# Kernel optimization log

Measured on AMD Instinct MI355X. Metric: run time of the kernel, lower is better.

## Reference

```python
import jax, jax.numpy as jnp
import numpy as np

N, E, G, H = 5000, 50000, 8, 4
GAT_DIMS = [(1536, 1024), (1024, 512), (512, 256)]
MLP_DIMS = [(256, 128), (128, 64), (64, 32), (32, 16), (16, 1)]
GATE_DIMS = [(256, 128), (128, 1)]
NEG_SLOPE = 0.2
EPS = 1e-16


def setup_inputs() -> dict:
    key = jax.random.key(0)
    keys = iter(jax.random.split(key, 80))

    def nrm(shape, s=0.05):
        return jax.random.normal(next(keys), shape, jnp.float32) * s

    inp = {}
    inp["x"] = jax.random.normal(next(keys), (N, 1536), jnp.float32)
    inp["edge_index"] = jax.random.randint(next(keys), (2, E), 0, N)
    inp["batch"] = jnp.sort(jax.random.randint(next(keys), (N,), 0, G))
    for i, (di, do) in enumerate(GAT_DIMS, 1):
        inp[f"Wl{i}"] = nrm((di, H * do))
        inp[f"bl{i}"] = jnp.zeros((H * do,), jnp.float32)
        inp[f"Wr{i}"] = nrm((di, H * do))
        inp[f"br{i}"] = jnp.zeros((H * do,), jnp.float32)
        inp[f"att{i}"] = nrm((H, do))
        inp[f"b{i}"] = jnp.zeros((do,), jnp.float32)
    for i, (di, do) in enumerate(MLP_DIMS):
        inp[f"Wm{i}"] = nrm((di, do))
        inp[f"bm{i}"] = jnp.zeros((do,), jnp.float32)
    for i, (di, do) in enumerate(GATE_DIMS):
        inp[f"Wg{i}"] = nrm((di, do))
        inp[f"bg{i}"] = jnp.zeros((do,), jnp.float32)
    return inp


def _gatv2(x, src, dst, Wl, bl, Wr, br, att, bias):
    # PyG GATv2Conv, concat=False: mean over heads.
    C = att.shape[1]
    xl = (x @ Wl + bl).reshape(-1, H, C)  # source-side transform [N,H,C]
    xr = (x @ Wr + br).reshape(-1, H, C)  # target-side transform [N,H,C]
    # edge scores: att . leaky_relu(x_j + x_i)  -> [E',H]
    s = jnp.sum(jax.nn.leaky_relu(xl[src] + xr[dst], negative_slope=NEG_SLOPE) * att, axis=-1)
    # segment softmax over destination node neighborhoods
    m = jax.ops.segment_max(s, dst, num_segments=N)
    ex = jnp.exp(s - m[dst])
    den = jax.ops.segment_sum(ex, dst, num_segments=N)
    alpha = ex / (den[dst] + EPS)
    out = jax.ops.segment_sum(alpha[:, :, None] * xl[src], dst, num_segments=N)  # [N,H,C]
    return out.mean(axis=1) + bias


def _forward(x, edge_index, batch, params):
    loop = jnp.arange(N)
    src = jnp.concatenate([edge_index[0], loop])  # add_self_loops=True (PyG default)
    dst = jnp.concatenate([edge_index[1], loop])
    for i in (1, 2, 3):
        x = jax.nn.relu(_gatv2(x, src, dst,
                               params[f"Wl{i}"], params[f"bl{i}"],
                               params[f"Wr{i}"], params[f"br{i}"],
                               params[f"att{i}"], params[f"b{i}"]))
    # AttentionalAggregation: segment-softmax(gate_nn(x)) weighted sum over graphs
    gate = jax.nn.relu(x @ params["Wg0"] + params["bg0"]) @ params["Wg1"] + params["bg1"]
    g = gate[:, 0]
    m = jax.ops.segment_max(g, batch, num_segments=G)
    ex = jnp.exp(g - m[batch])
    den = jax.ops.segment_sum(ex, batch, num_segments=G)
    w = ex / (den[batch] + EPS)
    h = jax.ops.segment_sum(w[:, None] * x, batch, num_segments=G)  # [G,256]
    for i in range(4):
        h = jax.nn.relu(h @ params[f"Wm{i}"] + params[f"bm{i}"])
    return h @ params["Wm4"] + params["bm4"]  # [G,1]


def reference(x, edge_index, batch,
              Wl1, bl1, Wr1, br1, att1, b1,
              Wl2, bl2, Wr2, br2, att2, b2,
              Wl3, bl3, Wr3, br3, att3, b3,
              Wm0, bm0, Wm1, bm1, Wm2, bm2, Wm3, bm3, Wm4, bm4,
              Wg0, bg0, Wg1, bg1):
    params = dict(locals())
    for k in ("x", "edge_index", "batch"):
        params.pop(k)
    return _forward(x, edge_index, batch, params)
```

## Files before the change

kernel.cpp:

```cpp
#include <hip/hip_runtime.h>
#include <math.h>

#define NN 5000
#define NNP 5120
#define NE 50000
#define NEE 55000
#define NG 8
#define NH 4

typedef __attribute__((ext_vector_type(8))) _Float16 half8;
typedef __attribute__((ext_vector_type(4))) _Float16 half4;
typedef __attribute__((ext_vector_type(4))) float floatx4;


__device__ inline float waveSum(float v) {
    #pragma unroll
    for (int o = 32; o > 0; o >>= 1) v += __shfl_xor(v, o, 64);
    return v;
}
__device__ inline float waveMax(float v) {
    #pragma unroll
    for (int o = 32; o > 0; o >>= 1) v = fmaxf(v, __shfl_xor(v, o, 64));
    return v;
}

__device__ __forceinline__ void gload_lds16(const _Float16* g, _Float16* l) {
    __builtin_amdgcn_global_load_lds(
        (__attribute__((address_space(1))) void*)g,
        (__attribute__((address_space(3))) void*)l,
        16, 0, 0);
}


__global__ void k_cvtA(const float* __restrict__ X, _Float16* __restrict__ A0, int n) {
    int i = blockIdx.x * 256 + threadIdx.x;
    if (i >= n) return;
    A0[i] = (_Float16)X[i];
}

__global__ __launch_bounds__(256) void k_cvtWT(const float* __restrict__ W,
        _Float16* __restrict__ B0, int K, int M)
{
    __shared__ float tile[32][33];
    int m0 = blockIdx.x * 32, k0 = blockIdx.y * 32;
    int tx = threadIdx.x & 31, ty = threadIdx.x >> 5;
    #pragma unroll
    for (int i = 0; i < 4; ++i)
        tile[ty + 8 * i][tx] = W[(size_t)(k0 + ty + 8 * i) * M + m0 + tx];
    __syncthreads();
    #pragma unroll
    for (int i = 0; i < 4; ++i) {
        int mm = ty + 8 * i, kk = tx;
        B0[(size_t)(m0 + mm) * K + kk + k0] = (_Float16)tile[kk][mm];
    }
}

__global__ __launch_bounds__(256) void gemm_mfma_f16(
    const _Float16* __restrict__ A0, const _Float16* __restrict__ B0,
    const float* __restrict__ bias, _Float16* __restrict__ C,
    int Mrows, int K, int N)
{
    __shared__ __align__(16) _Float16 As[2][128 * 32];
    __shared__ __align__(16) _Float16 Bs[2][128 * 32];

    const int tid = threadIdx.x;
    const int wave = tid >> 6;
    const int lane = tid & 63;
    const int wm = (wave >> 1) * 64;
    const int wn = (wave & 1) * 64;
    const int lm = lane & 15;
    const int kq = (lane >> 4) * 8;
    const int rowBase = blockIdx.y * 128;
    const int colBase = blockIdx.x * 128;

    floatx4 acc[4][4];
    #pragma unroll
    for (int i = 0; i < 4; ++i)
        #pragma unroll
        for (int j = 0; j < 4; ++j)
            acc[i][j] = (floatx4){0.f, 0.f, 0.f, 0.f};

    const int srow = wave * 32 + (lane >> 2);
    const int scol = (lane & 3) * 8;
    const _Float16* gA = A0 + (size_t)(rowBase + srow) * K + scol;
    const _Float16* gB = B0 + (size_t)(colBase + srow) * K + scol;
    const size_t rowSkip = (size_t)16 * K;
    const int lo0 = (wave * 32) * 32;
    const int lo1 = (wave * 32 + 16) * 32;

    gload_lds16(gA, &As[0][lo0]);
    gload_lds16(gA + rowSkip, &As[0][lo1]);
    gload_lds16(gB, &Bs[0][lo0]);
    gload_lds16(gB + rowSkip, &Bs[0][lo1]);
    __syncthreads();

    const int nk = K >> 5;
    for (int t = 0; t < nk; ++t) {
        const int p = t & 1;
        if (t + 1 < nk) {
            const int k1 = (t + 1) << 5;
            gload_lds16(gA + k1, &As[p ^ 1][lo0]);
            gload_lds16(gA + rowSkip + k1, &As[p ^ 1][lo1]);
            gload_lds16(gB + k1, &Bs[p ^ 1][lo0]);
            gload_lds16(gB + rowSkip + k1, &Bs[p ^ 1][lo1]);
        }
        half8 a0[4], b0[4];
        #pragma unroll
        for (int i = 0; i < 4; ++i) {
            a0[i] = *(const half8*)&As[p][(wm + i * 16 + lm) * 32 + kq];
            b0[i] = *(const half8*)&Bs[p][(wn + i * 16 + lm) * 32 + kq];
        }
        #pragma unroll
        for (int i = 0; i < 4; ++i)
            #pragma unroll
            for (int j = 0; j < 4; ++j)
                acc[i][j] = __builtin_amdgcn_mfma_f32_16x16x32_f16(a0[i], b0[j], acc[i][j], 0, 0, 0);
        __syncthreads();
    }

    const int cq = (lane >> 4) * 4;
    #pragma unroll
    for (int j = 0; j < 4; ++j) {
        int col = colBase + wn + j * 16 + lm;
        float bv = bias[col];
        #pragma unroll
        for (int i = 0; i < 4; ++i) {
            #pragma unroll
            for (int r = 0; r < 4; ++r) {
                int grow = rowBase + wm + i * 16 + cq + r;
                if (grow < Mrows)
                    C[(size_t)grow * N + col] = (_Float16)(acc[i][j][r] + bv);
            }
        }
    }
}


__global__ void k_build_edges(const int* __restrict__ ei, int* __restrict__ src,
                              int* __restrict__ dst) {
    int i = blockIdx.x * 256 + threadIdx.x;
    if (i < NE) { src[i] = ei[i]; dst[i] = ei[NE + i]; }
    else if (i < NEE) { src[i] = i - NE; dst[i] = i - NE; }
}

__global__ void k_zero32(unsigned int* __restrict__ p, int n) {
    int i = blockIdx.x * 256 + threadIdx.x;
    if (i < n) p[i] = 0u;
}

__global__ void k_count(const int* __restrict__ dst, int* __restrict__ cnt) {
    int i = blockIdx.x * 256 + threadIdx.x;
    if (i < NEE) atomicAdd(&cnt[dst[i]], 1);
}

__global__ __launch_bounds__(256) void k_scan(const int* __restrict__ cnt,
                                              int* __restrict__ off, int* __restrict__ cur) {
    __shared__ int partial[256];
    __shared__ int ppre[257];
    int t = threadIdx.x;
    const int chunk = (NN + 255) / 256;
    int lo = t * chunk, hi = min(NN, (t + 1) * chunk);
    int s = 0;
    for (int i = lo; i < hi; ++i) s += cnt[i];
    partial[t] = s;
    __syncthreads();
    if (t == 0) {
        int acc = 0;
        for (int i = 0; i < 256; ++i) { ppre[i] = acc; acc += partial[i]; }
        ppre[256] = acc;
    }
    __syncthreads();
    int acc = ppre[t];
    for (int i = lo; i < hi; ++i) { off[i] = acc; cur[i] = acc; acc += cnt[i]; }
    if (t == 0) off[NN] = ppre[256];
}

__global__ void k_fill(const int* __restrict__ src, const int* __restrict__ dst,
                       int* __restrict__ cur, int* __restrict__ slist) {
    int e = blockIdx.x * 256 + threadIdx.x;
    if (e < NEE) { int p = atomicAdd(&cur[dst[e]], 1); slist[p] = src[e]; }
}

template<int C>
__global__ __launch_bounds__(256) void k_gat_fused(
    const _Float16* __restrict__ xl, const _Float16* __restrict__ xr,
    const float* __restrict__ att, const int* __restrict__ eoff,
    const int* __restrict__ slist, const float* __restrict__ bias,
    _Float16* __restrict__ out)
{
    constexpr int NQ = C / 256;
    __shared__ float red[NH * C];
    const int n = blockIdx.x;
    const int h = threadIdx.x >> 6;
    const int lane = threadIdx.x & 63;

    float4 xr_reg[NQ], att_reg[NQ], acc[NQ];
    {
        const _Float16* xrow = xr + (size_t)n * (NH * C) + h * C;
        const float* ah   = att + h * C;
        #pragma unroll
        for (int q = 0; q < NQ; ++q) {
            int off = q * 256 + lane * 4;
            half4 hv = *(const half4*)(xrow + off);
            xr_reg[q] = make_float4((float)hv[0], (float)hv[1], (float)hv[2], (float)hv[3]);
            att_reg[q] = *(const float4*)(ah + off);
            acc[q] = make_float4(0.f, 0.f, 0.f, 0.f);
        }
    }
    float m = -INFINITY, den = 0.f;
    const int start = eoff[n], end = eoff[n + 1];

    for (int j = start; j < end; ++j) {
        int s = slist[j];
        const _Float16* xlr = xl + (size_t)s * (NH * C) + h * C;
        float4 xv[NQ];
        float ps = 0.f;
        #pragma unroll
        for (int q = 0; q < NQ; ++q) {
            half4 hv = *(const half4*)(xlr + q * 256 + lane * 4);
            xv[q] = make_float4((float)hv[0], (float)hv[1], (float)hv[2], (float)hv[3]);
            float vx = xv[q].x + xr_reg[q].x;
            float vy = xv[q].y + xr_reg[q].y;
            float vz = xv[q].z + xr_reg[q].z;
            float vw = xv[q].w + xr_reg[q].w;
            vx = vx > 0.f ? vx : 0.2f * vx;
            vy = vy > 0.f ? vy : 0.2f * vy;
            vz = vz > 0.f ? vz : 0.2f * vz;
            vw = vw > 0.f ? vw : 0.2f * vw;
            ps = fmaf(vx, att_reg[q].x, ps);
            ps = fmaf(vy, att_reg[q].y, ps);
            ps = fmaf(vz, att_reg[q].z, ps);
            ps = fmaf(vw, att_reg[q].w, ps);
        }
        ps = waveSum(ps);
        float m_new = fmaxf(m, ps);
        float scale = expf(m - m_new);
        float ex = expf(ps - m_new);
        den = den * scale + ex;
        m = m_new;
        #pragma unroll
        for (int q = 0; q < NQ; ++q) {
            acc[q].x = fmaf(ex, xv[q].x, acc[q].x * scale);
            acc[q].y = fmaf(ex, xv[q].y, acc[q].y * scale);
            acc[q].z = fmaf(ex, xv[q].z, acc[q].z * scale);
            acc[q].w = fmaf(ex, xv[q].w, acc[q].w * scale);
        }
    }

    float inv = 1.f / (den + 1e-16f);
    #pragma unroll
    for (int q = 0; q < NQ; ++q) {
        int off = q * 256 + lane * 4;
        float4 r;
        r.x = acc[q].x * inv; r.y = acc[q].y * inv;
        r.z = acc[q].z * inv; r.w = acc[q].w * inv;
        *(float4*)&red[h * C + off] = r;
    }
    __syncthreads();

    int t = threadIdx.x;
    for (int c4 = t; c4 < C / 4; c4 += 256) {
        int c = c4 * 4;
        float4 r0 = *(const float4*)&red[0 * C + c];
        float4 r1 = *(const float4*)&red[1 * C + c];
        float4 r2 = *(const float4*)&red[2 * C + c];
        float4 r3 = *(const float4*)&red[3 * C + c];
        float4 bv = *(const float4*)(bias + c);
        half4 o;
        o[0] = (_Float16)fmaxf((r0.x + r1.x + r2.x + r3.x) * 0.25f + bv.x, 0.f);
        o[1] = (_Float16)fmaxf((r0.y + r1.y + r2.y + r3.y) * 0.25f + bv.y, 0.f);
        o[2] = (_Float16)fmaxf((r0.z + r1.z + r2.z + r3.z) * 0.25f + bv.z, 0.f);
        o[3] = (_Float16)fmaxf((r0.w + r1.w + r2.w + r3.w) * 0.25f + bv.w, 0.f);
        *(half4*)(out + (size_t)n * C + c) = o;
    }
}


__global__ __launch_bounds__(128) void k_gate(
    const _Float16* __restrict__ x, const float* __restrict__ Wg0,
    const float* __restrict__ bg0, const float* __restrict__ Wg1,
    const float* __restrict__ bg1, float* __restrict__ g)
{
    int n = blockIdx.x;
    int t = threadIdx.x;
    __shared__ float xs[256];
    __shared__ float wsum[2];
    const _Float16* xp = x + (size_t)n * 256;
    xs[t] = (float)xp[t]; xs[t + 128] = (float)xp[t + 128];
    __syncthreads();
    float acc = bg0[t];
    for (int k = 0; k < 256; ++k) acc = fmaf(xs[k], Wg0[k * 128 + t], acc);
    acc = acc > 0.f ? acc : 0.f;
    float prod = acc * Wg1[t];
    prod = waveSum(prod);
    if ((t & 63) == 0) wsum[t >> 6] = prod;
    __syncthreads();
    if (t == 0) g[n] = wsum[0] + wsum[1] + bg1[0];
}

__global__ void k_group_bounds(const int* __restrict__ batch, int* __restrict__ gstart,
                               int* __restrict__ gend) {
    int n = blockIdx.x * 256 + threadIdx.x;
    if (n >= NN) return;
    int b = batch[n];
    if (n == 0 || batch[n - 1] != b) gstart[b] = n;
    if (n == NN - 1 || batch[n + 1] != b) gend[b] = n + 1;
}

__global__ __launch_bounds__(256) void k_pool_stats(
    const float* __restrict__ g, const int* __restrict__ gstart,
    const int* __restrict__ gend, float* __restrict__ mOut,
    float* __restrict__ invdenOut)
{
    int gi = blockIdx.x;
    int t = threadIdx.x;
    int s0 = gstart[gi], e0 = gend[gi];
    __shared__ float red[4];
    float mx = -1e30f;
    for (int n = s0 + t; n < e0; n += 256) mx = fmaxf(mx, g[n]);
    float wm = waveMax(mx);
    if ((t & 63) == 0) red[t >> 6] = wm;
    __syncthreads();
    float m = fmaxf(fmaxf(red[0], red[1]), fmaxf(red[2], red[3]));
    __syncthreads();
    float sm = 0.f;
    for (int n = s0 + t; n < e0; n += 256) sm += expf(g[n] - m);
    sm = waveSum(sm);
    if ((t & 63) == 0) red[t >> 6] = sm;
    __syncthreads();
    if (t == 0) {
        float den = red[0] + red[1] + red[2] + red[3] + 1e-16f;
        mOut[gi] = m;
        invdenOut[gi] = 1.f / den;
    }
}

#define PCH 16
__global__ __launch_bounds__(256) void k_pool_acc(
    const _Float16* __restrict__ x, const float* __restrict__ g,
    const int* __restrict__ batch, const float* __restrict__ m,
    const float* __restrict__ invden, float* __restrict__ hpool)
{
    int base = blockIdx.x * PCH;
    int t = threadIdx.x;
    float acc = 0.f;
    int cur = -1;
    for (int i = 0; i < PCH; ++i) {
        int n = base + i;
        if (n >= NN) break;
        int b = batch[n];
        if (b != cur) {
            if (cur >= 0) atomicAdd(&hpool[cur * 256 + t], acc);
            cur = b; acc = 0.f;
        }
        float w = expf(g[n] - m[b]) * invden[b];
        acc = fmaf(w, (float)x[(size_t)n * 256 + t], acc);
    }
    if (cur >= 0) atomicAdd(&hpool[cur * 256 + t], acc);
}

__global__ __launch_bounds__(256) void k_mlp(
    const float* __restrict__ hpool,
    const float* __restrict__ Wm0, const float* __restrict__ bm0,
    const float* __restrict__ Wm1, const float* __restrict__ bm1,
    const float* __restrict__ Wm2, const float* __restrict__ bm2,
    const float* __restrict__ Wm3, const float* __restrict__ bm3,
    const float* __restrict__ Wm4, const float* __restrict__ bm4,
    float* __restrict__ out)
{
    __shared__ float bufA[8 * 256];
    __shared__ float bufB[8 * 128];
    int t = threadIdx.x;
    for (int i = t; i < 8 * 256; i += 256) bufA[i] = hpool[i];
    __syncthreads();
    for (int i = t; i < 8 * 128; i += 256) {
        int r = i >> 7, c = i & 127;
        float acc = bm0[c];
        for (int k = 0; k < 256; ++k) acc = fmaf(bufA[r * 256 + k], Wm0[k * 128 + c], acc);
        bufB[i] = fmaxf(acc, 0.f);
    }
    __syncthreads();
    for (int i = t; i < 8 * 64; i += 256) {
        int r = i >> 6, c = i & 63;
        float acc = bm1[c];
        for (int k = 0; k < 128; ++k) acc = fmaf(bufB[r * 128 + k], Wm1[k * 64 + c], acc);
        bufA[i] = fmaxf(acc, 0.f);
    }
    __syncthreads();
    for (int i = t; i < 8 * 32; i += 256) {
        int r = i >> 5, c = i & 31;
        float acc = bm2[c];
        for (int k = 0; k < 64; ++k) acc = fmaf(bufA[r * 64 + k], Wm2[k * 32 + c], acc);
        bufB[i] = fmaxf(acc, 0.f);
    }
    __syncthreads();
    for (int i = t; i < 8 * 16; i += 256) {
        int r = i >> 4, c = i & 15;
        float acc = bm3[c];
        for (int k = 0; k < 32; ++k) acc = fmaf(bufB[r * 32 + k], Wm3[k * 16 + c], acc);
        bufA[i] = fmaxf(acc, 0.f);
    }
    __syncthreads();
    if (t < 8) {
        float acc = bm4[0];
        for (int k = 0; k < 16; ++k) acc = fmaf(bufA[t * 16 + k], Wm4[k], acc);
        out[t] = acc;
    }
}


static void run_gat_layer(const _Float16* ain, int K, int C,
                          const float* Wl, const float* bl,
                          const float* Wr, const float* br,
                          const float* att, const float* bias,
                          _Float16* wb0, _Float16* xl, _Float16* xr,
                          const int* eoff, const int* slist,
                          _Float16* xout, hipStream_t stream)
{
    int HC = NH * C;
    dim3 ggrid(HC / 128, NNP / 128);
    dim3 tgrid(HC / 32, K / 32);
    k_cvtWT<<<tgrid, 256, 0, stream>>>(Wl, wb0, K, HC);
    gemm_mfma_f16<<<ggrid, 256, 0, stream>>>(ain, wb0, bl, xl, NN, K, HC);
    k_cvtWT<<<tgrid, 256, 0, stream>>>(Wr, wb0, K, HC);
    gemm_mfma_f16<<<ggrid, 256, 0, stream>>>(ain, wb0, br, xr, NN, K, HC);

    if (C == 1024)
        k_gat_fused<1024><<<NN, 256, 0, stream>>>(xl, xr, att, eoff, slist, bias, xout);
    else if (C == 512)
        k_gat_fused<512><<<NN, 256, 0, stream>>>(xl, xr, att, eoff, slist, bias, xout);
    else
        k_gat_fused<256><<<NN, 256, 0, stream>>>(xl, xr, att, eoff, slist, bias, xout);
}

extern "C" void kernel_launch(void* const* d_in, const int* in_sizes, int n_in,
                              void* d_out, int out_size, void* d_ws, size_t ws_size,
                              hipStream_t stream) {
    const float* x      = (const float*)d_in[0];
    const int* ei       = (const int*)d_in[1];
    const int* batch    = (const int*)d_in[2];
    const float* Wl1 = (const float*)d_in[3];  const float* bl1 = (const float*)d_in[4];
    const float* Wr1 = (const float*)d_in[5];  const float* br1 = (const float*)d_in[6];
    const float* att1= (const float*)d_in[7];  const float* b1  = (const float*)d_in[8];
    const float* Wl2 = (const float*)d_in[9];  const float* bl2 = (const float*)d_in[10];
    const float* Wr2 = (const float*)d_in[11]; const float* br2 = (const float*)d_in[12];
    const float* att2= (const float*)d_in[13]; const float* b2  = (const float*)d_in[14];
    const float* Wl3 = (const float*)d_in[15]; const float* bl3 = (const float*)d_in[16];
    const float* Wr3 = (const float*)d_in[17]; const float* br3 = (const float*)d_in[18];
    const float* att3= (const float*)d_in[19]; const float* b3  = (const float*)d_in[20];
    const float* Wm0 = (const float*)d_in[21]; const float* bm0 = (const float*)d_in[22];
    const float* Wm1 = (const float*)d_in[23]; const float* bm1 = (const float*)d_in[24];
    const float* Wm2 = (const float*)d_in[25]; const float* bm2 = (const float*)d_in[26];
    const float* Wm3 = (const float*)d_in[27]; const float* bm3 = (const float*)d_in[28];
    const float* Wm4 = (const float*)d_in[29]; const float* bm4 = (const float*)d_in[30];
    const float* Wg0 = (const float*)d_in[31]; const float* bg0 = (const float*)d_in[32];
    const float* Wg1 = (const float*)d_in[33]; const float* bg1 = (const float*)d_in[34];
    float* out = (float*)d_out;

    float* ws = (float*)d_ws;
    size_t o = 0;
    _Float16* xl  = (_Float16*)(ws + o); o += (size_t)NNP * 4096 / 2;
    _Float16* xr  = (_Float16*)(ws + o); o += (size_t)NNP * 4096 / 2;
    _Float16* x1  = (_Float16*)(ws + o); o += (size_t)NNP * 1024 / 2;
    _Float16* x2  = (_Float16*)(ws + o); o += (size_t)NNP * 512 / 2;
    _Float16* x3  = (_Float16*)(ws + o); o += (size_t)NNP * 256 / 2;
    _Float16* a0p = (_Float16*)(ws + o); o += (size_t)NNP * 1536 / 2;
    _Float16* wb0 = (_Float16*)(ws + o); o += (size_t)1536 * 4096 / 2;
    int* srcA    = (int*)(ws + o); o += NEE;
    int* dstA    = (int*)(ws + o); o += NEE;
    int* cnt     = (int*)(ws + o); o += NN;
    int* eoff    = (int*)(ws + o); o += NN + 1;
    int* cur     = (int*)(ws + o); o += NN;
    int* slist   = (int*)(ws + o); o += NEE;
    float* g     = ws + o; o += NN;
    int* gstart  = (int*)(ws + o); o += NG;
    int* gend    = (int*)(ws + o); o += NG;
    float* gm    = ws + o; o += NG;
    float* ginv  = ws + o; o += NG;
    float* hpool = ws + o; o += NG * 256;

    int ebB = (NEE + 255) / 256;
    k_build_edges<<<ebB, 256, 0, stream>>>(ei, srcA, dstA);
    k_zero32<<<(NN + 255) / 256, 256, 0, stream>>>((unsigned int*)cnt, NN);
    k_count<<<ebB, 256, 0, stream>>>(dstA, cnt);
    k_scan<<<1, 256, 0, stream>>>(cnt, eoff, cur);
    k_fill<<<ebB, 256, 0, stream>>>(srcA, dstA, cur, slist);

    int nA = NN * 1536;
    k_cvtA<<<(nA + 255) / 256, 256, 0, stream>>>(x, a0p, nA);

    run_gat_layer(a0p, 1536, 1024, Wl1, bl1, Wr1, br1, att1, b1,
                  wb0, xl, xr, eoff, slist, x1, stream);
    run_gat_layer(x1,  1024, 512,  Wl2, bl2, Wr2, br2, att2, b2,
                  wb0, xl, xr, eoff, slist, x2, stream);
    run_gat_layer(x2,  512,  256,  Wl3, bl3, Wr3, br3, att3, b3,
                  wb0, xl, xr, eoff, slist, x3, stream);

    k_gate<<<NN, 128, 0, stream>>>(x3, Wg0, bg0, Wg1, bg1, g);
    k_zero32<<<1, 64, 0, stream>>>((unsigned int*)gstart, 2 * NG);
    k_group_bounds<<<(NN + 255) / 256, 256, 0, stream>>>(batch, gstart, gend);
    k_pool_stats<<<NG, 256, 0, stream>>>(g, gstart, gend, gm, ginv);
    k_zero32<<<(NG * 256 + 255) / 256, 256, 0, stream>>>((unsigned int*)hpool, NG * 256);
    k_pool_acc<<<(NN + PCH - 1) / PCH, 256, 0, stream>>>(x3, g, batch, gm, ginv, hpool);
    k_mlp<<<1, 256, 0, stream>>>(hpool, Wm0, bm0, Wm1, bm1, Wm2, bm2,
                                 Wm3, bm3, Wm4, bm4, out);
}
```

Before: 773.8 us.

## Fuse left/right projection GEMMs into one wide-tile GEMM and streamline GAT softmax

Concatenates the converted Wl and Wr weights so each layer runs a single GEMM producing an interleaved [xl|xr] buffer. The GEMM tile widens to 128x256 with 8 accumulators per row-tile and launch bounds of 2, so each A tile in LDS is reused across twice as many columns. The fused GAT kernel reads from the concatenated buffer with 16-byte half8 loads. The online softmax is split into a branch that skips the rescale when the score does not raise the running max, which saves one exp per edge on that path. The cost is doubled accumulator register pressure and LDS per block, which may reduce occupancy, plus a per-column branch to pick the bias.

Result: no change. 787.3 us (+1.7%).

```diff
diff --git a/kernel.cpp b/kernel.cpp
--- a/kernel.cpp
+++ b/kernel.cpp
@@ -55,74 +55,81 @@
     }
 }
 
-__global__ __launch_bounds__(256) void gemm_mfma_f16(
+__global__ __launch_bounds__(256, 2) void gemm_mfma_f16(
     const _Float16* __restrict__ A0, const _Float16* __restrict__ B0,
-    const float* __restrict__ bias, _Float16* __restrict__ C,
-    int Mrows, int K, int N)
+    const float* __restrict__ biasL, const float* __restrict__ biasR, int HC,
+    _Float16* __restrict__ C, int Mrows, int K, int N)
 {
     __shared__ __align__(16) _Float16 As[2][128 * 32];
-    __shared__ __align__(16) _Float16 Bs[2][128 * 32];
+    __shared__ __align__(16) _Float16 Bs[2][256 * 32];
 
     const int tid = threadIdx.x;
     const int wave = tid >> 6;
     const int lane = tid & 63;
     const int wm = (wave >> 1) * 64;
-    const int wn = (wave & 1) * 64;
+    const int wn = (wave & 1) * 128;
     const int lm = lane & 15;
     const int kq = (lane >> 4) * 8;
     const int rowBase = blockIdx.y * 128;
-    const int colBase = blockIdx.x * 128;
-
-    floatx4 acc[4][4];
+    const int colBase = blockIdx.x * 256;
+
+    floatx4 acc[4][8];
     #pragma unroll
     for (int i = 0; i < 4; ++i)
         #pragma unroll
-        for (int j = 0; j < 4; ++j)
+        for (int j = 0; j < 8; ++j)
             acc[i][j] = (floatx4){0.f, 0.f, 0.f, 0.f};
 
-    const int srow = wave * 32 + (lane >> 2);
+    const int sr = lane >> 2;
     const int scol = (lane & 3) * 8;
-    const _Float16* gA = A0 + (size_t)(rowBase + srow) * K + scol;
-    const _Float16* gB = B0 + (size_t)(colBase + srow) * K + scol;
-    const size_t rowSkip = (size_t)16 * K;
-    const int lo0 = (wave * 32) * 32;
-    const int lo1 = (wave * 32 + 16) * 32;
-
-    gload_lds16(gA, &As[0][lo0]);
-    gload_lds16(gA + rowSkip, &As[0][lo1]);
-    gload_lds16(gB, &Bs[0][lo0]);
-    gload_lds16(gB + rowSkip, &Bs[0][lo1]);
-    __syncthreads();
+    const _Float16* gA = A0 + (size_t)(rowBase + wave * 32 + sr) * K + scol;
+    const _Float16* gB = B0 + (size_t)(colBase + wave * 64 + sr) * K + scol;
+    const size_t skip16 = (size_t)16 * K;
+    const int loA = (wave * 32) * 32;
+    const int loB = (wave * 64) * 32;
 
     const int nk = K >> 5;
+    {
+        gload_lds16(gA, &As[0][loA]);
+        gload_lds16(gA + skip16, &As[0][loA + 16 * 32]);
+        gload_lds16(gB, &Bs[0][loB]);
+        gload_lds16(gB + skip16, &Bs[0][loB + 16 * 32]);
+        gload_lds16(gB + 2 * skip16, &Bs[0][loB + 32 * 32]);
+        gload_lds16(gB + 3 * skip16, &Bs[0][loB + 48 * 32]);
+    }
+    __syncthreads();
+
     for (int t = 0; t < nk; ++t) {
         const int p = t & 1;
         if (t + 1 < nk) {
             const int k1 = (t + 1) << 5;
-            gload_lds16(gA + k1, &As[p ^ 1][lo0]);
-            gload_lds16(gA + rowSkip + k1, &As[p ^ 1][lo1]);
-            gload_lds16(gB + k1, &Bs[p ^ 1][lo0]);
-            gload_lds16(gB + rowSkip + k1, &Bs[p ^ 1][lo1]);
-        }
-        half8 a0[4], b0[4];
-        #pragma unroll
-        for (int i = 0; i < 4; ++i) {
+            gload_lds16(gA + k1, &As[p ^ 1][loA]);
+            gload_lds16(gA + skip16 + k1, &As[p ^ 1][loA + 16 * 32]);
+            gload_lds16(gB + k1, &Bs[p ^ 1][loB]);
+            gload_lds16(gB + skip16 + k1, &Bs[p ^ 1][loB + 16 * 32]);
+            gload_lds16(gB + 2 * skip16 + k1, &Bs[p ^ 1][loB + 32 * 32]);
+            gload_lds16(gB + 3 * skip16 + k1, &Bs[p ^ 1][loB + 48 * 32]);
+        }
+        half8 a0[4], b0[8];
+        #pragma unroll
+        for (int i = 0; i < 4; ++i)
             a0[i] = *(const half8*)&As[p][(wm + i * 16 + lm) * 32 + kq];
-            b0[i] = *(const half8*)&Bs[p][(wn + i * 16 + lm) * 32 + kq];
-        }
+        #pragma unroll
+        for (int j = 0; j < 8; ++j)
+            b0[j] = *(const half8*)&Bs[p][(wn + j * 16 + lm) * 32 + kq];
         #pragma unroll
         for (int i = 0; i < 4; ++i)
             #pragma unroll
-            for (int j = 0; j < 4; ++j)
+            for (int j = 0; j < 8; ++j)
                 acc[i][j] = __builtin_amdgcn_mfma_f32_16x16x32_f16(a0[i], b0[j], acc[i][j], 0, 0, 0);
         __syncthreads();
     }
 
     const int cq = (lane >> 4) * 4;
     #pragma unroll
-    for (int j = 0; j < 4; ++j) {
+    for (int j = 0; j < 8; ++j) {
         int col = colBase + wn + j * 16 + lm;
-        float bv = bias[col];
+        float bv = (col < HC) ? biasL[col] : biasR[col - HC];
         #pragma unroll
         for (int i = 0; i < 4; ++i) {
             #pragma unroll
@@ -183,7 +190,7 @@
 
 template<int C>
 __global__ __launch_bounds__(256) void k_gat_fused(
-    const _Float16* __restrict__ xl, const _Float16* __restrict__ xr,
+    const _Float16* __restrict__ xcat,
     const float* __restrict__ att, const int* __restrict__ eoff,
     const int* __restrict__ slist, const float* __restrict__ bias,
     _Float16* __restrict__ out)
@@ -196,29 +203,49 @@
 
     float4 xr_reg[NQ], att_reg[NQ], acc[NQ];
     {
-        const _Float16* xrow = xr + (size_t)n * (NH * C) + h * C;
-        const float* ah   = att + h * C;
-        #pragma unroll
-        for (int q = 0; q < NQ; ++q) {
-            int off = q * 256 + lane * 4;
+        const _Float16* xrow = xcat + (size_t)n * (8 * C) + 4 * C + h * C;
+        const float* ah = att + h * C;
+        if constexpr (NQ >= 2) {
+            #pragma unroll
+            for (int q2 = 0; q2 < NQ / 2; ++q2) {
+                int off = q2 * 512 + lane * 8;
+                half8 hv = *(const half8*)(xrow + off);
+                xr_reg[2 * q2]     = make_float4((float)hv[0], (float)hv[1], (float)hv[2], (float)hv[3]);
+                xr_reg[2 * q2 + 1] = make_float4((float)hv[4], (float)hv[5], (float)hv[6], (float)hv[7]);
+                att_reg[2 * q2]     = *(const float4*)(ah + off);
+                att_reg[2 * q2 + 1] = *(const float4*)(ah + off + 4);
+            }
+        } else {
+            int off = lane * 4;
             half4 hv = *(const half4*)(xrow + off);
-            xr_reg[q] = make_float4((float)hv[0], (float)hv[1], (float)hv[2], (float)hv[3]);
-            att_reg[q] = *(const float4*)(ah + off);
-            acc[q] = make_float4(0.f, 0.f, 0.f, 0.f);
-        }
+            xr_reg[0] = make_float4((float)hv[0], (float)hv[1], (float)hv[2], (float)hv[3]);
+            att_reg[0] = *(const float4*)(ah + off);
+        }
+        #pragma unroll
+        for (int q = 0; q < NQ; ++q) acc[q] = make_float4(0.f, 0.f, 0.f, 0.f);
     }
     float m = -INFINITY, den = 0.f;
     const int start = eoff[n], end = eoff[n + 1];
 
     for (int j = start; j < end; ++j) {
         int s = slist[j];
-        const _Float16* xlr = xl + (size_t)s * (NH * C) + h * C;
+        const _Float16* xlr = xcat + (size_t)s * (8 * C) + h * C;
         float4 xv[NQ];
         float ps = 0.f;
+        if constexpr (NQ >= 2) {
+            #pragma unroll
+            for (int q2 = 0; q2 < NQ / 2; ++q2) {
+                int off = q2 * 512 + lane * 8;
+                half8 hv = *(const half8*)(xlr + off);
+                xv[2 * q2]     = make_float4((float)hv[0], (float)hv[1], (float)hv[2], (float)hv[3]);
+                xv[2 * q2 + 1] = make_float4((float)hv[4], (float)hv[5], (float)hv[6], (float)hv[7]);
+            }
+        } else {
+            half4 hv = *(const half4*)(xlr + lane * 4);
+            xv[0] = make_float4((float)hv[0], (float)hv[1], (float)hv[2], (float)hv[3]);
+        }
         #pragma unroll
         for (int q = 0; q < NQ; ++q) {
-            half4 hv = *(const half4*)(xlr + q * 256 + lane * 4);
-            xv[q] = make_float4((float)hv[0], (float)hv[1], (float)hv[2], (float)hv[3]);
             float vx = xv[q].x + xr_reg[q].x;
             float vy = xv[q].y + xr_reg[q].y;
             float vz = xv[q].z + xr_reg[q].z;
@@ -233,27 +260,48 @@
             ps = fmaf(vw, att_reg[q].w, ps);
         }
         ps = waveSum(ps);
-        float m_new = fmaxf(m, ps);
-        float scale = expf(m - m_new);
-        float ex = expf(ps - m_new);
-        den = den * scale + ex;
-        m = m_new;
-        #pragma unroll
-        for (int q = 0; q < NQ; ++q) {
-            acc[q].x = fmaf(ex, xv[q].x, acc[q].x * scale);
-            acc[q].y = fmaf(ex, xv[q].y, acc[q].y * scale);
-            acc[q].z = fmaf(ex, xv[q].z, acc[q].z * scale);
-            acc[q].w = fmaf(ex, xv[q].w, acc[q].w * scale);
+        if (ps <= m) {
+            float ex = expf(ps - m);
+            den += ex;
+            #pragma unroll
+            for (int q = 0; q < NQ; ++q) {
+                acc[q].x = fmaf(ex, xv[q].x, acc[q].x);
+                acc[q].y = fmaf(ex, xv[q].y, acc[q].y);
+                acc[q].z = fmaf(ex, xv[q].z, acc[q].z);
+                acc[q].w = fmaf(ex, xv[q].w, acc[q].w);
+            }
+        } else {
+            float scale = expf(m - ps);
+            den = den * scale + 1.f;
+            m = ps;
+            #pragma unroll
+            for (int q = 0; q < NQ; ++q) {
+                acc[q].x = fmaf(acc[q].x, scale, xv[q].x);
+                acc[q].y = fmaf(acc[q].y, scale, xv[q].y);
+                acc[q].z = fmaf(acc[q].z, scale, xv[q].z);
+                acc[q].w = fmaf(acc[q].w, scale, xv[q].w);
+            }
         }
     }
 
     float inv = 1.f / (den + 1e-16f);
-    #pragma unroll
-    for (int q = 0; q < NQ; ++q) {
-        int off = q * 256 + lane * 4;
+    if constexpr (NQ >= 2) {
+        #pragma unroll
+        for (int q2 = 0; q2 < NQ / 2; ++q2) {
+            int off = q2 * 512 + lane * 8;
+            float4 r0, r1;
+            r0.x = acc[2*q2].x * inv;   r0.y = acc[2*q2].y * inv;
+            r0.z = acc[2*q2].z * inv;   r0.w = acc[2*q2].w * inv;
+            r1.x = acc[2*q2+1].x * inv; r1.y = acc[2*q2+1].y * inv;
+            r1.z = acc[2*q2+1].z * inv; r1.w = acc[2*q2+1].w * inv;
+            *(float4*)&red[h * C + off] = r0;
+            *(float4*)&red[h * C + off + 4] = r1;
+        }
+    } else {
+        int off = lane * 4;
         float4 r;
-        r.x = acc[q].x * inv; r.y = acc[q].y * inv;
-        r.z = acc[q].z * inv; r.w = acc[q].w * inv;
+        r.x = acc[0].x * inv; r.y = acc[0].y * inv;
+        r.z = acc[0].z * inv; r.w = acc[0].w * inv;
         *(float4*)&red[h * C + off] = r;
     }
     __syncthreads();
@@ -413,24 +461,24 @@
                           const float* Wl, const float* bl,
                           const float* Wr, const float* br,
                           const float* att, const float* bias,
-                          _Float16* wb0, _Float16* xl, _Float16* xr,
+                          _Float16* wbcat, _Float16* xcat,
                           const int* eoff, const int* slist,
                           _Float16* xout, hipStream_t stream)
 {
     int HC = NH * C;
-    dim3 ggrid(HC / 128, NNP / 128);
     dim3 tgrid(HC / 32, K / 32);
-    k_cvtWT<<<tgrid, 256, 0, stream>>>(Wl, wb0, K, HC);
-    gemm_mfma_f16<<<ggrid, 256, 0, stream>>>(ain, wb0, bl, xl, NN, K, HC);
-    k_cvtWT<<<tgrid, 256, 0, stream>>>(Wr, wb0, K, HC);
-    gemm_mfma_f16<<<ggrid, 256, 0, stream>>>(ain, wb0, br, xr, NN, K, HC);
+    k_cvtWT<<<tgrid, 256, 0, stream>>>(Wl, wbcat, K, HC);
+    k_cvtWT<<<tgrid, 256, 0, stream>>>(Wr, wbcat + (size_t)HC * K, K, HC);
+    dim3 ggrid((2 * HC) / 256, NNP / 128);
+    gemm_mfma_f16<<<ggrid, 256, 0, stream>>>(ain, wbcat, bl, br, HC,
+                                             xcat, NN, K, 2 * HC);
 
     if (C == 1024)
-        k_gat_fused<1024><<<NN, 256, 0, stream>>>(xl, xr, att, eoff, slist, bias, xout);
+        k_gat_fused<1024><<<NN, 256, 0, stream>>>(xcat, att, eoff, slist, bias, xout);
     else if (C == 512)
-        k_gat_fused<512><<<NN, 256, 0, stream>>>(xl, xr, att, eoff, slist, bias, xout);
+        k_gat_fused<512><<<NN, 256, 0, stream>>>(xcat, att, eoff, slist, bias, xout);
     else
-        k_gat_fused<256><<<NN, 256, 0, stream>>>(xl, xr, att, eoff, slist, bias, xout);
+        k_gat_fused<256><<<NN, 256, 0, stream>>>(xcat, att, eoff, slist, bias, xout);
 }
 
 extern "C" void kernel_launch(void* const* d_in, const int* in_sizes, int n_in,
@@ -459,13 +507,12 @@
 
     float* ws = (float*)d_ws;
     size_t o = 0;
-    _Float16* xl  = (_Float16*)(ws + o); o += (size_t)NNP * 4096 / 2;
-    _Float16* xr  = (_Float16*)(ws + o); o += (size_t)NNP * 4096 / 2;
+    _Float16* xcat = (_Float16*)(ws + o); o += (size_t)NNP * 8192 / 2;
     _Float16* x1  = (_Float16*)(ws + o); o += (size_t)NNP * 1024 / 2;
     _Float16* x2  = (_Float16*)(ws + o); o += (size_t)NNP * 512 / 2;
     _Float16* x3  = (_Float16*)(ws + o); o += (size_t)NNP * 256 / 2;
     _Float16* a0p = (_Float16*)(ws + o); o += (size_t)NNP * 1536 / 2;
-    _Float16* wb0 = (_Float16*)(ws + o); o += (size_t)1536 * 4096 / 2;
+    _Float16* wbcat = (_Float16*)(ws + o); o += (size_t)2 * 1536 * 4096 / 2;
     int* srcA    = (int*)(ws + o); o += NEE;
     int* dstA    = (int*)(ws + o); o += NEE;
     int* cnt     = (int*)(ws + o); o += NN;
@@ -490,11 +537,11 @@
     k_cvtA<<<(nA + 255) / 256, 256, 0, stream>>>(x, a0p, nA);
 
     run_gat_layer(a0p, 1536, 1024, Wl1, bl1, Wr1, br1, att1, b1,
-                  wb0, xl, xr, eoff, slist, x1, stream);
+                  wbcat, xcat, eoff, slist, x1, stream);
     run_gat_layer(x1,  1024, 512,  Wl2, bl2, Wr2, br2, att2, b2,
-                  wb0, xl, xr, eoff, slist, x2, stream);
+                  wbcat, xcat, eoff, slist, x2, stream);
     run_gat_layer(x2,  512,  256,  Wl3, bl3, Wr3, br3, att3, b3,
-                  wb0, xl, xr, eoff, slist, x3, stream);
+                  wbcat, xcat, eoff, slist, x3, stream);
 
     k_gate<<<NN, 128, 0, stream>>>(x3, Wg0, bg0, Wg1, bg1, g);
     k_zero32<<<1, 64, 0, stream>>>((unsigned int*)gstart, 2 * NG);
```
